# Performance work log

Hardware: AMD Instinct MI355X
Metric: run time of the kernel (lower is better)

Reference implementation:

```python
import jax, jax.numpy as jnp
import numpy as np

N = 50000          # nodes
E = 800000         # edges (avg degree 16)
IN_C = 3
HEADS = 4
NUM_GRAPHS = 8
NUM_CLASSES = 10


def setup_inputs() -> dict:
    key = jax.random.key(0)
    ks = jax.random.split(key, 12)
    x = jax.random.normal(ks[0], (N, IN_C), jnp.float32)
    edge_index = jax.random.randint(ks[1], (2, E), 0, N, dtype=jnp.int64)
    batch = jnp.sort(jax.random.randint(ks[2], (N,), 0, NUM_GRAPHS, dtype=jnp.int64))

    def glorot(k, shape, fan):
        return jax.random.normal(k, shape, jnp.float32) * np.float32(1.0 / np.sqrt(fan))

    return {
        "x": x, "edge_index": edge_index, "batch": batch,
        "fc0_w": glorot(ks[3], (IN_C, 16), IN_C), "fc0_b": jnp.zeros((16,), jnp.float32),
        "u1": glorot(ks[4], (16, HEADS), 16), "c1": jnp.zeros((HEADS,), jnp.float32),
        "w1": glorot(ks[5], (16, HEADS * 32), 16), "b1": jnp.zeros((32,), jnp.float32),
        "u2": glorot(ks[6], (32, HEADS), 32), "c2": jnp.zeros((HEADS,), jnp.float32),
        "w2": glorot(ks[7], (32, HEADS * 64), 32), "b2": jnp.zeros((64,), jnp.float32),
        "fc1_w": glorot(ks[8], (64, NUM_CLASSES), 64), "fc1_b": jnp.zeros((NUM_CLASSES,), jnp.float32),
    }


def feast_conv(x, src, dst, u, c, w, b, heads, out_c):
    """FeaStConv (t_inv=True): per-edge head softmax on (x_j - x_i), mean aggregation."""
    n = x.shape[0]
    # soft-assignment over heads: [E, H]
    q = jax.nn.softmax((x[src] - x[dst]) @ u + c, axis=-1)
    # transform at node level, then gather per edge: [E, H, out_c]
    xw = (x @ w).reshape(n, heads, out_c)
    msg = jnp.einsum('eh,ehc->ec', q, xw[src])           # [E, out_c]
    agg = jax.ops.segment_sum(msg, dst, num_segments=n)  # sum over incoming edges
    cnt = jax.ops.segment_sum(jnp.ones((src.shape[0],), x.dtype), dst, num_segments=n)
    return agg / jnp.maximum(cnt, 1.0)[:, None] + b


def global_mean_pool(x, batch, num_graphs):
    s = jax.ops.segment_sum(x, batch, num_segments=num_graphs)
    cnt = jax.ops.segment_sum(jnp.ones((x.shape[0],), x.dtype), batch, num_segments=num_graphs)
    return s / jnp.maximum(cnt, 1.0)[:, None]


def reference(x, edge_index, batch, fc0_w, fc0_b, u1, c1, w1, b1, u2, c2, w2, b2, fc1_w, fc1_b):
    src, dst = edge_index[0], edge_index[1]   # x_j = x[src], x_i = x[dst]
    h = jax.nn.relu(x @ fc0_w + fc0_b)                              # [N, 16]
    h = jax.nn.relu(feast_conv(h, src, dst, u1, c1, w1, b1, HEADS, 32))  # [N, 32]
    h = jax.nn.relu(feast_conv(h, src, dst, u2, c2, w2, b2, HEADS, 64))  # [N, 64]
    g = global_mean_pool(h, batch, NUM_GRAPHS)                      # [G, 64]
    # dropout is identity in eval mode
    return g @ fc1_w + fc1_b                                        # [G, num_classes]
```

## Files before the change

### kernel.cpp

```cpp
#include <hip/hip_runtime.h>

#define N_NODES 50000
#define N_EDGES 800000
#define HEADS 4
#define NUM_GRAPHS 8

#define EBLK ((N_EDGES + 255) / 256)
#define NBLK ((N_NODES + 255) / 256)

__global__ __launch_bounds__(256) void hist_fc0_kernel(
    const int* __restrict__ dst, int* __restrict__ deg, int* __restrict__ off,
    const float* __restrict__ x,
    const float* __restrict__ fc0_w, const float* __restrict__ fc0_b,
    const float* __restrict__ u1,
    float* __restrict__ h0, float* __restrict__ P1) {
  if (blockIdx.x < EBLK) {
    int e = blockIdx.x * 256 + threadIdx.x;
    if (e < N_EDGES) off[e] = atomicAdd(&deg[dst[e]], 1);
    return;
  }
  __shared__ float sW0[3 * 16];
  __shared__ float sB0[16];
  __shared__ float sU[16 * 4];
  for (int i = threadIdx.x; i < 48; i += 256) sW0[i] = fc0_w[i];
  for (int i = threadIdx.x; i < 16; i += 256) sB0[i] = fc0_b[i];
  for (int i = threadIdx.x; i < 64; i += 256) sU[i] = u1[i];
  __syncthreads();
  int n = (blockIdx.x - EBLK) * 256 + threadIdx.x;
  if (n >= N_NODES) return;
  float x0 = x[n * 3 + 0], x1 = x[n * 3 + 1], x2 = x[n * 3 + 2];
  float h[16];
#pragma unroll
  for (int j = 0; j < 16; j++) {
    float v = x0 * sW0[0 * 16 + j] + x1 * sW0[1 * 16 + j] + x2 * sW0[2 * 16 + j] + sB0[j];
    h[j] = fmaxf(v, 0.f);
    h0[(size_t)n * 16 + j] = h[j];
  }
  float p0 = 0.f, p1 = 0.f, p2 = 0.f, p3 = 0.f;
#pragma unroll
  for (int j = 0; j < 16; j++) {
    p0 += h[j] * sU[j * 4 + 0];
    p1 += h[j] * sU[j * 4 + 1];
    p2 += h[j] * sU[j * 4 + 2];
    p3 += h[j] * sU[j * 4 + 3];
  }
  reinterpret_cast<float4*>(P1)[n] = make_float4(p0, p1, p2, p3);
}

__global__ __launch_bounds__(256) void alloc_kernel(const int* __restrict__ deg,
                                                    int* __restrict__ gctr,
                                                    int* __restrict__ rowstart) {
  int i = blockIdx.x * blockDim.x + threadIdx.x;
  int lane = threadIdx.x & 63;
  int d = (i < N_NODES) ? deg[i] : 0;
  int pre = d;
#pragma unroll
  for (int offd = 1; offd < 64; offd <<= 1) {
    int v = __shfl_up(pre, offd, 64);
    if (lane >= offd) pre += v;
  }
  int total = __shfl(pre, 63, 64);
  int base = 0;
  if (lane == 63) base = atomicAdd(gctr, total);
  base = __shfl(base, 63, 64);
  if (i < N_NODES) rowstart[i] = base + pre - d;
}

__global__ __launch_bounds__(256) void scatter_kernel(const int* __restrict__ src,
                                                      const int* __restrict__ dst,
                                                      const int* __restrict__ rowstart,
                                                      const int* __restrict__ off,
                                                      int* __restrict__ src_perm) {
  int e = blockIdx.x * blockDim.x + threadIdx.x;
  if (e >= N_EDGES) return;
  src_perm[rowstart[dst[e]] + off[e]] = src[e];
}

__device__ __forceinline__ float4 edge_q(float4 Ps, float b0, float b1, float b2, float b3) {
  float l0 = Ps.x + b0, l1 = Ps.y + b1, l2 = Ps.z + b2, l3 = Ps.w + b3;
  float m = fmaxf(fmaxf(l0, l1), fmaxf(l2, l3));
  float e0 = __expf(l0 - m), e1 = __expf(l1 - m), e2 = __expf(l2 - m), e3 = __expf(l3 - m);
  float inv = 1.f / (e0 + e1 + e2 + e3);
  return make_float4(e0 * inv, e1 * inv, e2 * inv, e3 * inv);
}

__global__ __launch_bounds__(256) void agg1_kernel(
    const int* __restrict__ rowstart, const int* __restrict__ deg,
    const int* __restrict__ src_perm,
    const float* __restrict__ P1, const float* __restrict__ c1,
    const float* __restrict__ h0,
    float* __restrict__ A) {
  int wave = threadIdx.x >> 6;
  int lane = threadIdx.x & 63;
  int g = lane >> 4;
  int j = lane & 15;
  int node = blockIdx.x * 4 + wave;
  if (node >= N_NODES) return;
  float4 Pd = reinterpret_cast<const float4*>(P1)[node];
  float b0 = c1[0] - Pd.x, b1 = c1[1] - Pd.y, b2 = c1[2] - Pd.z, b3 = c1[3] - Pd.w;
  int e0 = rowstart[node];
  int e1 = e0 + deg[node];
  const float4* P4 = reinterpret_cast<const float4*>(P1);
  float a0 = 0.f, a1 = 0.f, a2 = 0.f, a3 = 0.f;
  int p = e0;
  for (; p + 16 <= e1; p += 16) {
    int sA = src_perm[p + 0 + g];
    int sB = src_perm[p + 4 + g];
    int sC = src_perm[p + 8 + g];
    int sD = src_perm[p + 12 + g];
    float4 PA = P4[sA];
    float4 PB = P4[sB];
    float4 PC = P4[sC];
    float4 PD = P4[sD];
    float fA = h0[(size_t)sA * 16 + j];
    float fB = h0[(size_t)sB * 16 + j];
    float fC = h0[(size_t)sC * 16 + j];
    float fD = h0[(size_t)sD * 16 + j];
    float4 qA = edge_q(PA, b0, b1, b2, b3);
    float4 qB = edge_q(PB, b0, b1, b2, b3);
    float4 qC = edge_q(PC, b0, b1, b2, b3);
    float4 qD = edge_q(PD, b0, b1, b2, b3);
    a0 += qA.x * fA + qB.x * fB + qC.x * fC + qD.x * fD;
    a1 += qA.y * fA + qB.y * fB + qC.y * fC + qD.y * fD;
    a2 += qA.z * fA + qB.z * fB + qC.z * fC + qD.z * fD;
    a3 += qA.w * fA + qB.w * fB + qC.w * fC + qD.w * fD;
  }
  for (; p + 4 <= e1; p += 4) {
    int s = src_perm[p + g];
    float4 Ps = P4[s];
    float f = h0[(size_t)s * 16 + j];
    float4 q = edge_q(Ps, b0, b1, b2, b3);
    a0 += q.x * f; a1 += q.y * f; a2 += q.z * f; a3 += q.w * f;
  }
  int rem = e1 - p;
  if (g < rem) {
    int s = src_perm[p + g];
    float4 Ps = P4[s];
    float f = h0[(size_t)s * 16 + j];
    float4 q = edge_q(Ps, b0, b1, b2, b3);
    a0 += q.x * f; a1 += q.y * f; a2 += q.z * f; a3 += q.w * f;
  }
  a0 += __shfl_xor(a0, 16, 64); a0 += __shfl_xor(a0, 32, 64);
  a1 += __shfl_xor(a1, 16, 64); a1 += __shfl_xor(a1, 32, 64);
  a2 += __shfl_xor(a2, 16, 64); a2 += __shfl_xor(a2, 32, 64);
  a3 += __shfl_xor(a3, 16, 64); a3 += __shfl_xor(a3, 32, 64);
  float o = (g == 0) ? a0 : (g == 1) ? a1 : (g == 2) ? a2 : a3;
  A[(size_t)node * 64 + lane] = o;
}

__global__ __launch_bounds__(256) void agg2_kernel(
    const int* __restrict__ rowstart, const int* __restrict__ deg,
    const int* __restrict__ src_perm,
    const float* __restrict__ P2, const float* __restrict__ c2,
    const float* __restrict__ h1,
    float* __restrict__ A) {
  int wave = threadIdx.x >> 6;
  int lane = threadIdx.x & 63;
  int g = lane >> 5;
  int j = lane & 31;
  int node = blockIdx.x * 4 + wave;
  if (node >= N_NODES) return;
  float4 Pd = reinterpret_cast<const float4*>(P2)[node];
  float b0 = c2[0] - Pd.x, b1 = c2[1] - Pd.y, b2 = c2[2] - Pd.z, b3 = c2[3] - Pd.w;
  int e0 = rowstart[node];
  int e1 = e0 + deg[node];
  const float4* P4 = reinterpret_cast<const float4*>(P2);
  float a0 = 0.f, a1 = 0.f, a2 = 0.f, a3 = 0.f;
  int p = e0;
  for (; p + 8 <= e1; p += 8) {
    int sA = src_perm[p + 0 + g];
    int sB = src_perm[p + 2 + g];
    int sC = src_perm[p + 4 + g];
    int sD = src_perm[p + 6 + g];
    float4 PA = P4[sA];
    float4 PB = P4[sB];
    float4 PC = P4[sC];
    float4 PD = P4[sD];
    float fA = h1[(size_t)sA * 32 + j];
    float fB = h1[(size_t)sB * 32 + j];
    float fC = h1[(size_t)sC * 32 + j];
    float fD = h1[(size_t)sD * 32 + j];
    float4 qA = edge_q(PA, b0, b1, b2, b3);
    float4 qB = edge_q(PB, b0, b1, b2, b3);
    float4 qC = edge_q(PC, b0, b1, b2, b3);
    float4 qD = edge_q(PD, b0, b1, b2, b3);
    a0 += qA.x * fA + qB.x * fB + qC.x * fC + qD.x * fD;
    a1 += qA.y * fA + qB.y * fB + qC.y * fC + qD.y * fD;
    a2 += qA.z * fA + qB.z * fB + qC.z * fC + qD.z * fD;
    a3 += qA.w * fA + qB.w * fB + qC.w * fC + qD.w * fD;
  }
  for (; p + 2 <= e1; p += 2) {
    int s = src_perm[p + g];
    float4 Ps = P4[s];
    float f = h1[(size_t)s * 32 + j];
    float4 q = edge_q(Ps, b0, b1, b2, b3);
    a0 += q.x * f; a1 += q.y * f; a2 += q.z * f; a3 += q.w * f;
  }
  int rem = e1 - p;
  if (g < rem) {
    int s = src_perm[p + g];
    float4 Ps = P4[s];
    float f = h1[(size_t)s * 32 + j];
    float4 q = edge_q(Ps, b0, b1, b2, b3);
    a0 += q.x * f; a1 += q.y * f; a2 += q.z * f; a3 += q.w * f;
  }
  a0 += __shfl_xor(a0, 32, 64);
  a1 += __shfl_xor(a1, 32, 64);
  a2 += __shfl_xor(a2, 32, 64);
  a3 += __shfl_xor(a3, 32, 64);
  float oa = (g == 0) ? a0 : a1;
  float ob = (g == 0) ? a2 : a3;
  A[(size_t)node * 128 + lane] = oa;
  A[(size_t)node * 128 + 64 + lane] = ob;
}

__global__ __launch_bounds__(256) void gemm1_kernel(
    const int* __restrict__ deg, const float* __restrict__ A,
    const float* __restrict__ w1, const float* __restrict__ b1,
    const float* __restrict__ u2,
    float* __restrict__ h1, float* __restrict__ P2) {
  __shared__ float sB[64 * 32];
  __shared__ float sU[32 * 4];
  for (int i = threadIdx.x; i < 64 * 32; i += 256) {
    int hj = i / 32, c = i % 32;
    sB[i] = w1[(hj % 16) * 128 + (hj / 16) * 32 + c];
  }
  for (int i = threadIdx.x; i < 128; i += 256) sU[i] = u2[i];
  __syncthreads();
  const float4* sB4 = reinterpret_cast<const float4*>(sB);
  int c4 = threadIdx.x & 7;
  int g = threadIdx.x >> 3;
  int n0 = blockIdx.x * 64 + g * 2;
  int n1 = n0 + 1;
  int na = min(n0, N_NODES - 1);
  int nb = min(n1, N_NODES - 1);
  const float4* A0 = reinterpret_cast<const float4*>(A + (size_t)na * 64);
  const float4* A1 = reinterpret_cast<const float4*>(A + (size_t)nb * 64);
  float4 bc = reinterpret_cast<const float4*>(b1)[c4];
  float4 acc0 = {0, 0, 0, 0}, acc1 = {0, 0, 0, 0};
#pragma unroll 2
  for (int k4 = 0; k4 < 16; k4++) {
    float4 a0 = A0[k4];
    float4 a1 = A1[k4];
    float4 w0 = sB4[(4 * k4 + 0) * 8 + c4];
    float4 wv1 = sB4[(4 * k4 + 1) * 8 + c4];
    float4 w2v = sB4[(4 * k4 + 2) * 8 + c4];
    float4 w3 = sB4[(4 * k4 + 3) * 8 + c4];
    acc0.x += a0.x * w0.x + a0.y * wv1.x + a0.z * w2v.x + a0.w * w3.x;
    acc0.y += a0.x * w0.y + a0.y * wv1.y + a0.z * w2v.y + a0.w * w3.y;
    acc0.z += a0.x * w0.z + a0.y * wv1.z + a0.z * w2v.z + a0.w * w3.z;
    acc0.w += a0.x * w0.w + a0.y * wv1.w + a0.z * w2v.w + a0.w * w3.w;
    acc1.x += a1.x * w0.x + a1.y * wv1.x + a1.z * w2v.x + a1.w * w3.x;
    acc1.y += a1.x * w0.y + a1.y * wv1.y + a1.z * w2v.y + a1.w * w3.y;
    acc1.z += a1.x * w0.z + a1.y * wv1.z + a1.z * w2v.z + a1.w * w3.z;
    acc1.w += a1.x * w0.w + a1.y * wv1.w + a1.z * w2v.w + a1.w * w3.w;
  }
  float inv0 = 1.f / fmaxf((float)deg[na], 1.f);
  float inv1 = 1.f / fmaxf((float)deg[nb], 1.f);
  float4 o0 = {fmaxf(acc0.x * inv0 + bc.x, 0.f), fmaxf(acc0.y * inv0 + bc.y, 0.f),
               fmaxf(acc0.z * inv0 + bc.z, 0.f), fmaxf(acc0.w * inv0 + bc.w, 0.f)};
  float4 o1 = {fmaxf(acc1.x * inv1 + bc.x, 0.f), fmaxf(acc1.y * inv1 + bc.y, 0.f),
               fmaxf(acc1.z * inv1 + bc.z, 0.f), fmaxf(acc1.w * inv1 + bc.w, 0.f)};
  if (n0 < N_NODES) reinterpret_cast<float4*>(h1 + (size_t)n0 * 32)[c4] = o0;
  if (n1 < N_NODES) reinterpret_cast<float4*>(h1 + (size_t)n1 * 32)[c4] = o1;
  float pa[4] = {0, 0, 0, 0}, pb[4] = {0, 0, 0, 0};
#pragma unroll
  for (int k = 0; k < 4; k++) {
    int c = 4 * c4 + k;
    float v0 = k == 0 ? o0.x : k == 1 ? o0.y : k == 2 ? o0.z : o0.w;
    float v1 = k == 0 ? o1.x : k == 1 ? o1.y : k == 2 ? o1.z : o1.w;
#pragma unroll
    for (int hh = 0; hh < 4; hh++) {
      pa[hh] += v0 * sU[c * 4 + hh];
      pb[hh] += v1 * sU[c * 4 + hh];
    }
  }
#pragma unroll
  for (int msk = 1; msk <= 4; msk <<= 1) {
#pragma unroll
    for (int hh = 0; hh < 4; hh++) {
      pa[hh] += __shfl_xor(pa[hh], msk, 64);
      pb[hh] += __shfl_xor(pb[hh], msk, 64);
    }
  }
  if (c4 == 0) {
    if (n0 < N_NODES)
      reinterpret_cast<float4*>(P2)[n0] = make_float4(pa[0], pa[1], pa[2], pa[3]);
    if (n1 < N_NODES)
      reinterpret_cast<float4*>(P2)[n1] = make_float4(pb[0], pb[1], pb[2], pb[3]);
  }
}

__global__ __launch_bounds__(256) void gemm2_pool_kernel(
    const int* __restrict__ deg, const float* __restrict__ A,
    const float* __restrict__ w2, const float* __restrict__ b2,
    const int* __restrict__ batch,
    float* __restrict__ gsum, float* __restrict__ gcnt) {
  __shared__ float sg[2][64];
  __shared__ float scnt[2];
  __shared__ int sgmin, sgmax;
  if (threadIdx.x < 128) sg[threadIdx.x >> 6][threadIdx.x & 63] = 0.f;
  if (threadIdx.x < 2) scnt[threadIdx.x] = 0.f;
  if (threadIdx.x == 0) {
    int base = (int)blockIdx.x * 32;
    int last = base + 31;
    if (last > N_NODES - 1) last = N_NODES - 1;
    sgmin = batch[base];
    sgmax = batch[last];
  }
  __syncthreads();
  const float4* W4 = reinterpret_cast<const float4*>(w2);
  int c4 = threadIdx.x & 15;
  int g = threadIdx.x >> 4;
  int n0 = (int)blockIdx.x * 32 + g * 2;
  int n1 = n0 + 1;
  int na = min(n0, N_NODES - 1);
  int nb = min(n1, N_NODES - 1);
  const float4* A0 = reinterpret_cast<const float4*>(A + (size_t)na * 128);
  const float4* A1 = reinterpret_cast<const float4*>(A + (size_t)nb * 128);
  float4 bc = reinterpret_cast<const float4*>(b2)[c4];
  float4 acc0 = {0, 0, 0, 0}, acc1 = {0, 0, 0, 0};
#pragma unroll 2
  for (int k4 = 0; k4 < 32; k4++) {
    float4 a0 = A0[k4];
    float4 a1 = A1[k4];
    int k0 = 4 * k4;
    float4 w0 = W4[((k0 + 0) & 31) * 64 + ((k0 + 0) >> 5) * 16 + c4];
    float4 wv1 = W4[((k0 + 1) & 31) * 64 + ((k0 + 1) >> 5) * 16 + c4];
    float4 w2v = W4[((k0 + 2) & 31) * 64 + ((k0 + 2) >> 5) * 16 + c4];
    float4 w3 = W4[((k0 + 3) & 31) * 64 + ((k0 + 3) >> 5) * 16 + c4];
    acc0.x += a0.x * w0.x + a0.y * wv1.x + a0.z * w2v.x + a0.w * w3.x;
    acc0.y += a0.x * w0.y + a0.y * wv1.y + a0.z * w2v.y + a0.w * w3.y;
    acc0.z += a0.x * w0.z + a0.y * wv1.z + a0.z * w2v.z + a0.w * w3.z;
    acc0.w += a0.x * w0.w + a0.y * wv1.w + a0.z * w2v.w + a0.w * w3.w;
    acc1.x += a1.x * w0.x + a1.y * wv1.x + a1.z * w2v.x + a1.w * w3.x;
    acc1.y += a1.x * w0.y + a1.y * wv1.y + a1.z * w2v.y + a1.w * w3.y;
    acc1.z += a1.x * w0.z + a1.y * wv1.z + a1.z * w2v.z + a1.w * w3.z;
    acc1.w += a1.x * w0.w + a1.y * wv1.w + a1.z * w2v.w + a1.w * w3.w;
  }
  float inv0 = 1.f / fmaxf((float)deg[na], 1.f);
  float inv1 = 1.f / fmaxf((float)deg[nb], 1.f);
  float4 o0 = {fmaxf(acc0.x * inv0 + bc.x, 0.f), fmaxf(acc0.y * inv0 + bc.y, 0.f),
               fmaxf(acc0.z * inv0 + bc.z, 0.f), fmaxf(acc0.w * inv0 + bc.w, 0.f)};
  float4 o1 = {fmaxf(acc1.x * inv1 + bc.x, 0.f), fmaxf(acc1.y * inv1 + bc.y, 0.f),
               fmaxf(acc1.z * inv1 + bc.z, 0.f), fmaxf(acc1.w * inv1 + bc.w, 0.f)};
  int gmin = sgmin;
  if (n0 < N_NODES) {
    int b0v = batch[na];
    int slot = b0v - gmin;
    if (slot <= 1) {
      atomicAdd(&sg[slot][c4 * 4 + 0], o0.x);
      atomicAdd(&sg[slot][c4 * 4 + 1], o0.y);
      atomicAdd(&sg[slot][c4 * 4 + 2], o0.z);
      atomicAdd(&sg[slot][c4 * 4 + 3], o0.w);
      if (c4 == 0) atomicAdd(&scnt[slot], 1.f);
    } else {
      atomicAdd(&gsum[b0v * 64 + c4 * 4 + 0], o0.x);
      atomicAdd(&gsum[b0v * 64 + c4 * 4 + 1], o0.y);
      atomicAdd(&gsum[b0v * 64 + c4 * 4 + 2], o0.z);
      atomicAdd(&gsum[b0v * 64 + c4 * 4 + 3], o0.w);
      if (c4 == 0) atomicAdd(&gcnt[b0v], 1.f);
    }
  }
  if (n1 < N_NODES) {
    int b1v = batch[nb];
    int slot = b1v - gmin;
    if (slot <= 1) {
      atomicAdd(&sg[slot][c4 * 4 + 0], o1.x);
      atomicAdd(&sg[slot][c4 * 4 + 1], o1.y);
      atomicAdd(&sg[slot][c4 * 4 + 2], o1.z);
      atomicAdd(&sg[slot][c4 * 4 + 3], o1.w);
      if (c4 == 0) atomicAdd(&scnt[slot], 1.f);
    } else {
      atomicAdd(&gsum[b1v * 64 + c4 * 4 + 0], o1.x);
      atomicAdd(&gsum[b1v * 64 + c4 * 4 + 1], o1.y);
      atomicAdd(&gsum[b1v * 64 + c4 * 4 + 2], o1.z);
      atomicAdd(&gsum[b1v * 64 + c4 * 4 + 3], o1.w);
      if (c4 == 0) atomicAdd(&gcnt[b1v], 1.f);
    }
  }
  __syncthreads();
  if (threadIdx.x < 128) {
    int slot = threadIdx.x >> 6, ch = threadIdx.x & 63;
    if (slot == 0 || sgmax > sgmin) {
      int gg = sgmin + slot;
      atomicAdd(&gsum[gg * 64 + ch], sg[slot][ch]);
      if (ch == 0) atomicAdd(&gcnt[gg], scnt[slot]);
    }
  }
}

__global__ __launch_bounds__(128) void head_kernel(
    const float* __restrict__ gsum, const float* __restrict__ gcnt,
    const float* __restrict__ fc1_w, const float* __restrict__ fc1_b,
    float* __restrict__ out) {
  int t = threadIdx.x;
  if (t >= NUM_GRAPHS * 10) return;
  int g = t / 10, k = t % 10;
  float inv = 1.f / fmaxf(gcnt[g], 1.f);
  float s = fc1_b[k];
#pragma unroll
  for (int c = 0; c < 64; c++) s += gsum[g * 64 + c] * inv * fc1_w[c * 10 + k];
  out[g * 10 + k] = s;
}

extern "C" void kernel_launch(void* const* d_in, const int* in_sizes, int n_in,
                              void* d_out, int out_size, void* d_ws, size_t ws_size,
                              hipStream_t stream) {
  const float* x = (const float*)d_in[0];
  const int* edge_index = (const int*)d_in[1];
  const int* batch = (const int*)d_in[2];
  const float* fc0_w = (const float*)d_in[3];
  const float* fc0_b = (const float*)d_in[4];
  const float* u1 = (const float*)d_in[5];
  const float* c1 = (const float*)d_in[6];
  const float* w1 = (const float*)d_in[7];
  const float* b1 = (const float*)d_in[8];
  const float* u2 = (const float*)d_in[9];
  const float* c2 = (const float*)d_in[10];
  const float* w2 = (const float*)d_in[11];
  const float* b2 = (const float*)d_in[12];
  const float* fc1_w = (const float*)d_in[13];
  const float* fc1_b = (const float*)d_in[14];
  float* out = (float*)d_out;

  const int* src = edge_index;
  const int* dst = edge_index + N_EDGES;

  char* wsb = (char*)d_ws;
  int* deg = (int*)wsb;
  int* gctr = deg + N_NODES;
  float* gsum = (float*)wsb + 50004;
  float* gcnt = gsum + NUM_GRAPHS * 64;
  int* rowstart = (int*)wsb + 50524;
  int* off = rowstart + N_NODES;
  int* src_perm = off + N_EDGES;
  float* h0 = (float*)wsb + 1700524;
  float* h1 = h0 + (size_t)N_NODES * 16;
  float* A = h1 + (size_t)N_NODES * 32;
  float* P1 = A + (size_t)N_NODES * 128;
  float* P2 = P1 + (size_t)N_NODES * 4;

  (void)hipMemsetAsync(d_ws, 0, 50524 * sizeof(int), stream);

  int nblk = NBLK;
  int eblk = EBLK;
  int wblk = (N_NODES + 3) / 4;

  hist_fc0_kernel<<<eblk + nblk, 256, 0, stream>>>(dst, deg, off, x, fc0_w, fc0_b, u1, h0, P1);
  alloc_kernel<<<nblk, 256, 0, stream>>>(deg, gctr, rowstart);
  scatter_kernel<<<eblk, 256, 0, stream>>>(src, dst, rowstart, off, src_perm);

  agg1_kernel<<<wblk, 256, 0, stream>>>(rowstart, deg, src_perm, P1, c1, h0, A);
  gemm1_kernel<<<(N_NODES + 63) / 64, 256, 0, stream>>>(deg, A, w1, b1, u2, h1, P2);

  agg2_kernel<<<wblk, 256, 0, stream>>>(rowstart, deg, src_perm, P2, c2, h1, A);
  gemm2_pool_kernel<<<(N_NODES + 31) / 32, 256, 0, stream>>>(deg, A, w2, b2, batch, gsum, gcnt);
  head_kernel<<<1, 128, 0, stream>>>(gsum, gcnt, fc1_w, fc1_b, out);
}
```

Baseline: 272.7 us.

## Restructure gemm2_pool to stage A rows in LDS with one output channel per lane

The second-layer GEMM+pool kernel now assigns each wave two nodes and each lane one of the 64 output channels. The two A rows are staged in shared memory with coalesced float4 loads and then broadcast-read, and w2 is read as scalar values coalesced across lanes. The grid grows from 32 to 8 nodes per block, which gives many more blocks and waves in flight. The cost is more w2 traffic per node, since it is re-read by every wave, and bounds guards are dropped because the code relies on N_NODES being divisible by 8.

```diff
diff --git a/kernel.cpp b/kernel.cpp
--- a/kernel.cpp
+++ b/kernel.cpp
@@ -296,88 +296,65 @@
     const float* __restrict__ w2, const float* __restrict__ b2,
     const int* __restrict__ batch,
     float* __restrict__ gsum, float* __restrict__ gcnt) {
+  __shared__ float lsA[4][2][128];
   __shared__ float sg[2][64];
   __shared__ float scnt[2];
   __shared__ int sgmin, sgmax;
+  int wave = threadIdx.x >> 6;
+  int lane = threadIdx.x & 63;
   if (threadIdx.x < 128) sg[threadIdx.x >> 6][threadIdx.x & 63] = 0.f;
   if (threadIdx.x < 2) scnt[threadIdx.x] = 0.f;
   if (threadIdx.x == 0) {
-    int base = (int)blockIdx.x * 32;
-    int last = base + 31;
-    if (last > N_NODES - 1) last = N_NODES - 1;
+    int base = (int)blockIdx.x * 8;
     sgmin = batch[base];
-    sgmax = batch[last];
-  }
+    sgmax = batch[base + 7];
+  }
+  int n0 = (int)blockIdx.x * 8 + wave * 2;
+  int n1 = n0 + 1;
+  int r = lane >> 5;
+  int c4i = lane & 31;
+  float4 av = reinterpret_cast<const float4*>(A)[(size_t)(n0 + r) * 32 + c4i];
+  reinterpret_cast<float4*>(&lsA[wave][r][0])[c4i] = av;
   __syncthreads();
-  const float4* W4 = reinterpret_cast<const float4*>(w2);
-  int c4 = threadIdx.x & 15;
-  int g = threadIdx.x >> 4;
-  int n0 = (int)blockIdx.x * 32 + g * 2;
-  int n1 = n0 + 1;
-  int na = min(n0, N_NODES - 1);
-  int nb = min(n1, N_NODES - 1);
-  const float4* A0 = reinterpret_cast<const float4*>(A + (size_t)na * 128);
-  const float4* A1 = reinterpret_cast<const float4*>(A + (size_t)nb * 128);
-  float4 bc = reinterpret_cast<const float4*>(b2)[c4];
-  float4 acc0 = {0, 0, 0, 0}, acc1 = {0, 0, 0, 0};
+  float accA = 0.f, accB = 0.f;
+  const float4* a0p = reinterpret_cast<const float4*>(&lsA[wave][0][0]);
+  const float4* a1p = reinterpret_cast<const float4*>(&lsA[wave][1][0]);
+#pragma unroll
+  for (int h = 0; h < 4; h++) {
+    const float* wp = w2 + h * 64 + lane;
 #pragma unroll 2
-  for (int k4 = 0; k4 < 32; k4++) {
-    float4 a0 = A0[k4];
-    float4 a1 = A1[k4];
-    int k0 = 4 * k4;
-    float4 w0 = W4[((k0 + 0) & 31) * 64 + ((k0 + 0) >> 5) * 16 + c4];
-    float4 wv1 = W4[((k0 + 1) & 31) * 64 + ((k0 + 1) >> 5) * 16 + c4];
-    float4 w2v = W4[((k0 + 2) & 31) * 64 + ((k0 + 2) >> 5) * 16 + c4];
-    float4 w3 = W4[((k0 + 3) & 31) * 64 + ((k0 + 3) >> 5) * 16 + c4];
-    acc0.x += a0.x * w0.x + a0.y * wv1.x + a0.z * w2v.x + a0.w * w3.x;
-    acc0.y += a0.x * w0.y + a0.y * wv1.y + a0.z * w2v.y + a0.w * w3.y;
-    acc0.z += a0.x * w0.z + a0.y * wv1.z + a0.z * w2v.z + a0.w * w3.z;
-    acc0.w += a0.x * w0.w + a0.y * wv1.w + a0.z * w2v.w + a0.w * w3.w;
-    acc1.x += a1.x * w0.x + a1.y * wv1.x + a1.z * w2v.x + a1.w * w3.x;
-    acc1.y += a1.x * w0.y + a1.y * wv1.y + a1.z * w2v.y + a1.w * w3.y;
-    acc1.z += a1.x * w0.z + a1.y * wv1.z + a1.z * w2v.z + a1.w * w3.z;
-    acc1.w += a1.x * w0.w + a1.y * wv1.w + a1.z * w2v.w + a1.w * w3.w;
-  }
-  float inv0 = 1.f / fmaxf((float)deg[na], 1.f);
-  float inv1 = 1.f / fmaxf((float)deg[nb], 1.f);
-  float4 o0 = {fmaxf(acc0.x * inv0 + bc.x, 0.f), fmaxf(acc0.y * inv0 + bc.y, 0.f),
-               fmaxf(acc0.z * inv0 + bc.z, 0.f), fmaxf(acc0.w * inv0 + bc.w, 0.f)};
-  float4 o1 = {fmaxf(acc1.x * inv1 + bc.x, 0.f), fmaxf(acc1.y * inv1 + bc.y, 0.f),
-               fmaxf(acc1.z * inv1 + bc.z, 0.f), fmaxf(acc1.w * inv1 + bc.w, 0.f)};
-  int gmin = sgmin;
-  if (n0 < N_NODES) {
-    int b0v = batch[na];
-    int slot = b0v - gmin;
-    if (slot <= 1) {
-      atomicAdd(&sg[slot][c4 * 4 + 0], o0.x);
-      atomicAdd(&sg[slot][c4 * 4 + 1], o0.y);
-      atomicAdd(&sg[slot][c4 * 4 + 2], o0.z);
-      atomicAdd(&sg[slot][c4 * 4 + 3], o0.w);
-      if (c4 == 0) atomicAdd(&scnt[slot], 1.f);
-    } else {
-      atomicAdd(&gsum[b0v * 64 + c4 * 4 + 0], o0.x);
-      atomicAdd(&gsum[b0v * 64 + c4 * 4 + 1], o0.y);
-      atomicAdd(&gsum[b0v * 64 + c4 * 4 + 2], o0.z);
-      atomicAdd(&gsum[b0v * 64 + c4 * 4 + 3], o0.w);
-      if (c4 == 0) atomicAdd(&gcnt[b0v], 1.f);
+    for (int q8 = 0; q8 < 8; q8++) {
+      float4 a0 = a0p[h * 8 + q8];
+      float4 a1 = a1p[h * 8 + q8];
+      int cb = q8 * 4;
+      float w0 = wp[(cb + 0) * 256];
+      float w1v = wp[(cb + 1) * 256];
+      float w2v = wp[(cb + 2) * 256];
+      float w3 = wp[(cb + 3) * 256];
+      accA += a0.x * w0 + a0.y * w1v + a0.z * w2v + a0.w * w3;
+      accB += a1.x * w0 + a1.y * w1v + a1.z * w2v + a1.w * w3;
     }
   }
-  if (n1 < N_NODES) {
-    int b1v = batch[nb];
-    int slot = b1v - gmin;
-    if (slot <= 1) {
-      atomicAdd(&sg[slot][c4 * 4 + 0], o1.x);
-      atomicAdd(&sg[slot][c4 * 4 + 1], o1.y);
-      atomicAdd(&sg[slot][c4 * 4 + 2], o1.z);
-      atomicAdd(&sg[slot][c4 * 4 + 3], o1.w);
-      if (c4 == 0) atomicAdd(&scnt[slot], 1.f);
-    } else {
-      atomicAdd(&gsum[b1v * 64 + c4 * 4 + 0], o1.x);
-      atomicAdd(&gsum[b1v * 64 + c4 * 4 + 1], o1.y);
-      atomicAdd(&gsum[b1v * 64 + c4 * 4 + 2], o1.z);
-      atomicAdd(&gsum[b1v * 64 + c4 * 4 + 3], o1.w);
-      if (c4 == 0) atomicAdd(&gcnt[b1v], 1.f);
-    }
+  float bcv = b2[lane];
+  float inv0 = 1.f / fmaxf((float)deg[n0], 1.f);
+  float inv1 = 1.f / fmaxf((float)deg[n1], 1.f);
+  float h2a = fmaxf(accA * inv0 + bcv, 0.f);
+  float h2b = fmaxf(accB * inv1 + bcv, 0.f);
+  int b0v = batch[n0], b1v = batch[n1];
+  int s0 = b0v - sgmin, s1 = b1v - sgmin;
+  if (s0 <= 1) {
+    atomicAdd(&sg[s0][lane], h2a);
+    if (lane == 0) atomicAdd(&scnt[s0], 1.f);
+  } else {
+    atomicAdd(&gsum[b0v * 64 + lane], h2a);
+    if (lane == 0) atomicAdd(&gcnt[b0v], 1.f);
+  }
+  if (s1 <= 1) {
+    atomicAdd(&sg[s1][lane], h2b);
+    if (lane == 0) atomicAdd(&scnt[s1], 1.f);
+  } else {
+    atomicAdd(&gsum[b1v * 64 + lane], h2b);
+    if (lane == 0) atomicAdd(&gcnt[b1v], 1.f);
   }
   __syncthreads();
   if (threadIdx.x < 128) {
@@ -455,6 +432,6 @@
   gemm1_kernel<<<(N_NODES + 63) / 64, 256, 0, stream>>>(deg, A, w1, b1, u2, h1, P2);
 
   agg2_kernel<<<wblk, 256, 0, stream>>>(rowstart, deg, src_perm, P2, c2, h1, A);
-  gemm2_pool_kernel<<<(N_NODES + 31) / 32, 256, 0, stream>>>(deg, A, w2, b2, batch, gsum, gcnt);
+  gemm2_pool_kernel<<<N_NODES / 8, 256, 0, stream>>>(deg, A, w2, b2, batch, gsum, gcnt);
   head_kernel<<<1, 128, 0, stream>>>(gsum, gcnt, fc1_w, fc1_b, out);
 }
```

After: 329.8 us. 1.21x slower.
